# Kernel tuning notes

Measured on AMD Instinct MI355X. Metric: run time of the kernel, lower is better.

## Reference

```python
import jax, jax.numpy as jnp
import numpy as np

NEG_SLOPE = 0.2

def gat_conv(x, src, dst, n, W, a_src, a_dst, b):
    # PyG GATConv, heads=1: h = xW; e_ij = LeakyReLU(a_src.h_j + a_dst.h_i)
    # alpha = softmax over incoming edges of i; out_i = sum_j alpha_ij * h_j + b
    h = x @ W                               # [N, F_out]
    s_src = h @ a_src                       # [N]
    s_dst = h @ a_dst                       # [N]
    e = s_src[src] + s_dst[dst]             # [E]
    e = jnp.where(e > 0, e, NEG_SLOPE * e)  # leaky relu
    # numerically stable scatter-softmax over destination groups
    m = jax.ops.segment_max(e, dst, num_segments=n)          # [N]
    ee = jnp.exp(e - m[dst])                                  # [E]
    denom = jax.ops.segment_sum(ee, dst, num_segments=n)      # [N]
    alpha = ee / denom[dst]                                    # [E]
    out = jax.ops.segment_sum(alpha[:, None] * h[src], dst, num_segments=n)
    return out + b

def add_self_loops(edge_index, n):
    loops = jnp.arange(n, dtype=edge_index.dtype)
    src = jnp.concatenate([edge_index[0], loops])
    dst = jnp.concatenate([edge_index[1], loops])
    return src, dst

def setup_inputs() -> dict:
    key = jax.random.key(0)
    ks = jax.random.split(key, 12)
    N, E, F_IN, H1, H2, C = 50000, 800000, 1433, 512, 256, 7
    x = jax.random.normal(ks[0], (N, F_IN), dtype=jnp.float32)
    edge_index = jax.random.randint(ks[1], (2, E), 0, N, dtype=jnp.int64)
    def glorot(k, shape):
        lim = float(np.sqrt(6.0 / (shape[0] + shape[-1])))
        return jax.random.uniform(k, shape, jnp.float32, -lim, lim)
    params = {
        'W1': glorot(ks[2], (F_IN, H1)), 'as1': glorot(ks[3], (H1,)), 'ad1': glorot(ks[4], (H1,)), 'b1': jnp.zeros((H1,), jnp.float32),
        'W2': glorot(ks[5], (H1, H2)), 'as2': glorot(ks[6], (H2,)), 'ad2': glorot(ks[7], (H2,)), 'b2': jnp.zeros((H2,), jnp.float32),
        'W3': glorot(ks[8], (H2, C)), 'as3': glorot(ks[9], (C,)), 'ad3': glorot(ks[10], (C,)), 'b3': jnp.zeros((C,), jnp.float32),
    }
    return {'x': x, 'edge_index': edge_index, **params}

def reference(x, edge_index, W1, as1, ad1, b1, W2, as2, ad2, b2, W3, as3, ad3, b3):
    n = x.shape[0]
    src, dst = add_self_loops(edge_index, n)
    h = jax.nn.relu(gat_conv(x, src, dst, n, W1, as1, ad1, b1))
    h = jax.nn.relu(gat_conv(h, src, dst, n, W2, as2, ad2, b2))
    h = gat_conv(h, src, dst, n, W3, as3, ad3, b3)
    return jax.nn.log_softmax(h, axis=1)
```

## Files before the change

kernel.cpp:

```cpp
#include <hip/hip_runtime.h>
#include <hip/hip_bf16.h>
#include <math.h>

constexpr int N_NODES = 50000;
constexpr int E_EDGES = 800000;
constexpr int E_TOT   = E_EDGES + N_NODES;
constexpr int F_IN  = 1433;
constexpr int KPAD1 = 1440;
constexpr int F1 = 512;
constexpr int F2 = 256;
constexpr int NC = 7;
constexpr int MAXDEG = 1024;
constexpr float NEG_SLOPE = 0.2f;

typedef unsigned short u16;
typedef unsigned int   u32;
typedef short s16x8 __attribute__((ext_vector_type(8)));
typedef float f32x4 __attribute__((ext_vector_type(4)));
typedef float float4a __attribute__((ext_vector_type(4), aligned(4)));

__device__ inline u16 f2b(float f) {
    u32 u = __float_as_uint(f);
    u32 r = (u + 0x7fffu + ((u >> 16) & 1u)) >> 16;
    return (u16)r;
}
__device__ inline float b2f(u16 b) { return __uint_as_float(((u32)b) << 16); }

__device__ inline u32 pkbf16(float lo, float hi) {
    union { __hip_bfloat162 h; u32 u; } c;
    c.h = __float22bfloat162_rn(make_float2(lo, hi));
    return c.u;
}

__device__ inline void gload_lds16(const void* g, void* l) {
    __builtin_amdgcn_global_load_lds(
        (const __attribute__((address_space(1))) u32*)g,
        (__attribute__((address_space(3))) u32*)l, 16, 0, 0);
}

__device__ inline void loadA8(const float* p, int gk, float4a& v0, float4a& v1) {
    if (gk + 8 <= F_IN) {
        v0 = *(const float4a*)p;
        v1 = *(const float4a*)(p + 4);
    } else {
#pragma unroll
        for (int i = 0; i < 4; ++i) v0[i] = (gk + i < F_IN) ? p[i] : 0.f;
#pragma unroll
        for (int i = 0; i < 4; ++i) v1[i] = (gk + 4 + i < F_IN) ? p[4 + i] : 0.f;
    }
}

__global__ void count_dst_kernel(const int* __restrict__ dst, int* __restrict__ counts) {
    int i = blockIdx.x * blockDim.x + threadIdx.x;
    if (i < E_TOT) {
        int d = (i < E_EDGES) ? dst[i] : (i - E_EDGES);
        atomicAdd(&counts[d], 1);
    }
}

__global__ __launch_bounds__(1024) void scan_kernel(const int* __restrict__ counts,
                                                    int* __restrict__ row_ptr, int n) {
    __shared__ int part[1024];
    int t = threadIdx.x;
    int chunk = (n + 1023) / 1024;
    int lo = t * chunk;
    int hi = min(lo + chunk, n);
    int s = 0;
    for (int i = lo; i < hi; ++i) s += counts[i];
    part[t] = s;
    __syncthreads();
    for (int off = 1; off < 1024; off <<= 1) {
        int v = 0;
        if (t >= off) v = part[t - off];
        __syncthreads();
        part[t] += v;
        __syncthreads();
    }
    int run = part[t] - s;
    for (int i = lo; i < hi; ++i) { row_ptr[i] = run; run += counts[i]; }
    if (t == 1023) row_ptr[n] = part[1023];
}

__global__ void scatter_kernel(const int* __restrict__ src, const int* __restrict__ dst,
                               const int* __restrict__ row_ptr, int* __restrict__ fill,
                               int* __restrict__ col) {
    int i = blockIdx.x * blockDim.x + threadIdx.x;
    if (i < E_TOT) {
        int s = (i < E_EDGES) ? src[i] : (i - E_EDGES);
        int d = (i < E_EDGES) ? dst[i] : (i - E_EDGES);
        int p = row_ptr[d] + atomicAdd(&fill[d], 1);
        col[p] = s;
    }
}

__global__ void convert_wt_kernel(const float* __restrict__ W, u32* __restrict__ Wt,
                                  int K, int Nn, int KP) {
    int p = blockIdx.x * blockDim.x + threadIdx.x;
    int ppr = KP / 2;
    if (p >= Nn * ppr) return;
    int n = p / ppr;
    int k = (p - n * ppr) * 2;
    float v0 = (k + 0 < K) ? W[(size_t)(k + 0) * Nn + n] : 0.f;
    float v1 = (k + 1 < K) ? W[(size_t)(k + 1) * Nn + n] : 0.f;
    Wt[p] = (u32)f2b(v0) | ((u32)f2b(v1) << 16);
}

__global__ __launch_bounds__(256, 2) void gemm1_fused(const float* __restrict__ A,
                                                      const u16* __restrict__ Bt,
                                                      u16* __restrict__ C) {
    constexpr int M = N_NODES;
    constexpr int ABUF = 64 * 32;
    constexpr int BBUF = 512 * 32;
    __shared__ u16 sA[2 * ABUF];
    __shared__ u16 sB[2 * BBUF];
    int tid  = threadIdx.x;
    int wave = tid >> 6;
    int lane = tid & 63;
    int quad = lane >> 4;
    int lm   = lane & 15;
    int m0 = blockIdx.x * 64;

    int arow  = min(m0 + (tid >> 2), M - 1);
    int aslot = (tid & 3) ^ ((tid >> 3) & 3);
    const float* xcol = A + (size_t)arow * F_IN + aslot * 8;
    int acolbase = aslot * 8;

    const u16* gB[8];
    u16* lB[8];
#pragma unroll
    for (int c = 0; c < 8; ++c) {
        int chunk = wave * 8 + c;
        int row  = chunk * 16 + (lane >> 2);
        int slot = (lane & 3) ^ ((lane >> 3) & 3);
        gB[c] = Bt + (size_t)row * KPAD1 + slot * 8;
        lB[c] = &sB[chunk * 512];
    }

    f32x4 acc[4][8];
#pragma unroll
    for (int i = 0; i < 4; ++i)
#pragma unroll
        for (int j = 0; j < 8; ++j) acc[i][j] = (f32x4){0.f, 0.f, 0.f, 0.f};

    int rdoff = (quad ^ ((lm >> 1) & 3)) * 8;

    {
#pragma unroll
        for (int c = 0; c < 8; ++c) gload_lds16(gB[c], lB[c]);
        float4a a0, a1;
        loadA8(xcol, acolbase, a0, a1);
        uint4 pk;
        pk.x = pkbf16(a0[0], a0[1]); pk.y = pkbf16(a0[2], a0[3]);
        pk.z = pkbf16(a1[0], a1[1]); pk.w = pkbf16(a1[2], a1[3]);
        *(uint4*)&sA[tid * 8] = pk;
    }
    __syncthreads();

    int cur = 0;
    for (int k0 = 0; k0 < KPAD1; k0 += 32) {
        int kn = k0 + 32;
        bool hasnext = kn < KPAD1;
        int nxt = cur ^ 1;

        float4a a0, a1;
        if (hasnext) {
#pragma unroll
            for (int c = 0; c < 8; ++c) gload_lds16(gB[c] + kn, lB[c] + nxt * BBUF);
            loadA8(xcol + kn, acolbase + kn, a0, a1);
        }

        const u16* sAc = &sA[cur * ABUF];
        const u16* sBc = &sB[cur * BBUF];
        s16x8 af[4], bf[8];
#pragma unroll
        for (int mt = 0; mt < 4; ++mt)
            af[mt] = *(const s16x8*)&sAc[(mt * 16 + lm) * 32 + rdoff];
#pragma unroll
        for (int nt = 0; nt < 8; ++nt)
            bf[nt] = *(const s16x8*)&sBc[(wave * 128 + nt * 16 + lm) * 32 + rdoff];
#pragma unroll
        for (int mt = 0; mt < 4; ++mt)
#pragma unroll
            for (int nt = 0; nt < 8; ++nt)
                acc[mt][nt] = __builtin_amdgcn_mfma_f32_16x16x32_bf16(
                    af[mt], bf[nt], acc[mt][nt], 0, 0, 0);

        if (hasnext) {
            uint4 pk;
            pk.x = pkbf16(a0[0], a0[1]); pk.y = pkbf16(a0[2], a0[3]);
            pk.z = pkbf16(a1[0], a1[1]); pk.w = pkbf16(a1[2], a1[3]);
            *(uint4*)&sA[nxt * ABUF + tid * 8] = pk;
        }
        __syncthreads();
        cur = nxt;
    }

#pragma unroll
    for (int mt = 0; mt < 4; ++mt) {
        int mbase = m0 + mt * 16 + quad * 4;
#pragma unroll
        for (int nt = 0; nt < 8; ++nt) {
            int n = wave * 128 + nt * 16 + lm;
#pragma unroll
            for (int r = 0; r < 4; ++r) {
                int m = mbase + r;
                if (m < M) C[(size_t)m * F1 + n] = f2b(acc[mt][nt][r]);
            }
        }
    }
}

__global__ __launch_bounds__(256) void mfma_gemm_bt(const u16* __restrict__ A,
                                                    const u16* __restrict__ Bt,
                                                    u16* __restrict__ C,
                                                    int M, int N, int K) {
    __shared__ u16 sA[128 * 32];
    __shared__ u16 sB[128 * 32];
    int tid  = threadIdx.x;
    int wave = tid >> 6;
    int lane = tid & 63;
    int quad = lane >> 4;
    int lm   = lane & 15;
    int wm = wave & 1;
    int wn = wave >> 1;
    int m0 = blockIdx.y * 128;
    int n0 = blockIdx.x * 128;

    int ch0 = wave * 2, ch1 = wave * 2 + 1;
    int rsub = lane >> 2;
    int csub = (lane & 3) * 8;
    int ar0 = min(m0 + ch0 * 16 + rsub, M - 1);
    int ar1 = min(m0 + ch1 * 16 + rsub, M - 1);
    int br0 = n0 + ch0 * 16 + rsub;
    int br1 = n0 + ch1 * 16 + rsub;
    const u16* gA0 = A + (size_t)ar0 * K + csub;
    const u16* gA1 = A + (size_t)ar1 * K + csub;
    const u16* gB0 = Bt + (size_t)br0 * K + csub;
    const u16* gB1 = Bt + (size_t)br1 * K + csub;

    f32x4 acc[4][4];
#pragma unroll
    for (int i = 0; i < 4; ++i)
#pragma unroll
        for (int j = 0; j < 4; ++j) acc[i][j] = (f32x4){0.f, 0.f, 0.f, 0.f};

    for (int k0 = 0; k0 < K; k0 += 32) {
        gload_lds16(gA0 + k0, &sA[ch0 * 512]);
        gload_lds16(gA1 + k0, &sA[ch1 * 512]);
        gload_lds16(gB0 + k0, &sB[ch0 * 512]);
        gload_lds16(gB1 + k0, &sB[ch1 * 512]);
        __syncthreads();

        s16x8 af[4], bf[4];
#pragma unroll
        for (int mt = 0; mt < 4; ++mt)
            af[mt] = *(const s16x8*)&sA[(wm * 64 + mt * 16 + lm) * 32 + quad * 8];
#pragma unroll
        for (int nt = 0; nt < 4; ++nt)
            bf[nt] = *(const s16x8*)&sB[(wn * 64 + nt * 16 + lm) * 32 + quad * 8];
#pragma unroll
        for (int mt = 0; mt < 4; ++mt)
#pragma unroll
            for (int nt = 0; nt < 4; ++nt)
                acc[mt][nt] = __builtin_amdgcn_mfma_f32_16x16x32_bf16(
                    af[mt], bf[nt], acc[mt][nt], 0, 0, 0);
        __syncthreads();
    }

#pragma unroll
    for (int mt = 0; mt < 4; ++mt) {
        int mbase = m0 + wm * 64 + mt * 16 + quad * 4;
#pragma unroll
        for (int nt = 0; nt < 4; ++nt) {
            int n = n0 + wn * 64 + nt * 16 + lm;
#pragma unroll
            for (int r = 0; r < 4; ++r) {
                int m = mbase + r;
                if (m < M) C[(size_t)m * N + n] = f2b(acc[mt][nt][r]);
            }
        }
    }
}

template <int F>
__global__ __launch_bounds__(256) void scores_bf16_kernel(const u16* __restrict__ h,
                                                          const float* __restrict__ a_src,
                                                          const float* __restrict__ a_dst,
                                                          float* __restrict__ s_src,
                                                          float* __restrict__ s_dst, int n) {
    int gwid = (blockIdx.x * blockDim.x + threadIdx.x) >> 6;
    int lane = threadIdx.x & 63;
    if (gwid >= n) return;
    const u32* row = (const u32*)(h + (size_t)gwid * F);
    float acc1 = 0.f, acc2 = 0.f;
    for (int p = lane; p < F / 2; p += 64) {
        u32 u = row[p];
        float v0 = b2f((u16)(u & 0xffff));
        float v1 = b2f((u16)(u >> 16));
        acc1 += v0 * a_src[2 * p] + v1 * a_src[2 * p + 1];
        acc2 += v0 * a_dst[2 * p] + v1 * a_dst[2 * p + 1];
    }
#pragma unroll
    for (int o = 32; o; o >>= 1) {
        acc1 += __shfl_xor(acc1, o);
        acc2 += __shfl_xor(acc2, o);
    }
    if (lane == 0) { s_src[gwid] = acc1; s_dst[gwid] = acc2; }
}

template <int F>
__global__ __launch_bounds__(256) void scores_kernel(const float* __restrict__ h,
                                                     const float* __restrict__ a_src,
                                                     const float* __restrict__ a_dst,
                                                     float* __restrict__ s_src,
                                                     float* __restrict__ s_dst, int n) {
    int gwid = (blockIdx.x * blockDim.x + threadIdx.x) >> 6;
    int lane = threadIdx.x & 63;
    if (gwid >= n) return;
    const float* row = h + (size_t)gwid * F;
    float acc1 = 0.f, acc2 = 0.f;
    for (int f = lane; f < F; f += 64) {
        float v = row[f];
        acc1 += v * a_src[f];
        acc2 += v * a_dst[f];
    }
#pragma unroll
    for (int o = 32; o; o >>= 1) {
        acc1 += __shfl_xor(acc1, o);
        acc2 += __shfl_xor(acc2, o);
    }
    if (lane == 0) { s_src[gwid] = acc1; s_dst[gwid] = acc2; }
}

template <int F, bool OUT_BF16>
__global__ __launch_bounds__(256) void agg_gather_kernel(const u16* __restrict__ h,
                                                         const float* __restrict__ s_src,
                                                         const float* __restrict__ s_dst,
                                                         const float* __restrict__ bias,
                                                         const int* __restrict__ row_ptr,
                                                         const int* __restrict__ col,
                                                         void* __restrict__ out) {
    constexpr int UPL = F / 128;
    int node = blockIdx.x;
    int tid = threadIdx.x;
    int wave = tid >> 6;
    int lane = tid & 63;
    int beg = row_ptr[node];
    int deg = min(row_ptr[node + 1] - beg, MAXDEG);

    __shared__ float w[MAXDEG];
    __shared__ int cs[MAXDEG];
    __shared__ float sdenom;
    __shared__ float red[4][F];

    if (wave == 0) {
        float sd = s_dst[node];
        float m = -1e30f;
        for (int j = lane; j < deg; j += 64) {
            int s = col[beg + j];
            cs[j] = s;
            float e = s_src[s] + sd;
            e = (e > 0.f) ? e : NEG_SLOPE * e;
            w[j] = e;
            m = fmaxf(m, e);
        }
#pragma unroll
        for (int o = 32; o; o >>= 1) m = fmaxf(m, __shfl_xor(m, o));
        float sum = 0.f;
        for (int j = lane; j < deg; j += 64) {
            float v = expf(w[j] - m);
            w[j] = v;
            sum += v;
        }
#pragma unroll
        for (int o = 32; o; o >>= 1) sum += __shfl_xor(sum, o);
        if (lane == 0) sdenom = sum;
    }
    __syncthreads();
    float inv = 1.0f / sdenom;

    float acc[2 * UPL];
#pragma unroll
    for (int e = 0; e < 2 * UPL; ++e) acc[e] = 0.f;

    int j = wave;
    for (; j + 4 < deg; j += 8) {
        float wg0 = w[j] * inv;
        float wg1 = w[j + 4] * inv;
        const u32* r0 = (const u32*)(h + (size_t)cs[j] * F) + lane * UPL;
        const u32* r1 = (const u32*)(h + (size_t)cs[j + 4] * F) + lane * UPL;
        u32 v0[UPL], v1[UPL];
        if constexpr (UPL == 4) {
            uint4 q0 = *(const uint4*)r0; v0[0] = q0.x; v0[1] = q0.y; v0[2] = q0.z; v0[3] = q0.w;
            uint4 q1 = *(const uint4*)r1; v1[0] = q1.x; v1[1] = q1.y; v1[2] = q1.z; v1[3] = q1.w;
        } else {
            uint2 q0 = *(const uint2*)r0; v0[0] = q0.x; v0[1] = q0.y;
            uint2 q1 = *(const uint2*)r1; v1[0] = q1.x; v1[1] = q1.y;
        }
#pragma unroll
        for (int u = 0; u < UPL; ++u) {
            acc[2 * u]     += wg0 * b2f((u16)(v0[u] & 0xffff)) + wg1 * b2f((u16)(v1[u] & 0xffff));
            acc[2 * u + 1] += wg0 * b2f((u16)(v0[u] >> 16))    + wg1 * b2f((u16)(v1[u] >> 16));
        }
    }
    if (j < deg) {
        float wg = w[j] * inv;
        const u32* r = (const u32*)(h + (size_t)cs[j] * F) + lane * UPL;
        u32 v[UPL];
        if constexpr (UPL == 4) {
            uint4 q = *(const uint4*)r; v[0] = q.x; v[1] = q.y; v[2] = q.z; v[3] = q.w;
        } else {
            uint2 q = *(const uint2*)r; v[0] = q.x; v[1] = q.y;
        }
#pragma unroll
        for (int u = 0; u < UPL; ++u) {
            acc[2 * u]     += wg * b2f((u16)(v[u] & 0xffff));
            acc[2 * u + 1] += wg * b2f((u16)(v[u] >> 16));
        }
    }

#pragma unroll
    for (int e = 0; e < 2 * UPL; ++e) red[wave][lane * 2 * UPL + e] = acc[e];
    __syncthreads();

    if constexpr (OUT_BF16) {
        if (tid < F / 2) {
            int f = tid * 2;
            float v0 = red[0][f] + red[1][f] + red[2][f] + red[3][f] + bias[f];
            float v1 = red[0][f + 1] + red[1][f + 1] + red[2][f + 1] + red[3][f + 1] + bias[f + 1];
            v0 = fmaxf(v0, 0.f);
            v1 = fmaxf(v1, 0.f);
            ((u32*)out)[(size_t)node * (F / 2) + tid] = (u32)f2b(v0) | ((u32)f2b(v1) << 16);
        }
    } else {
        if (tid < F) {
            float v = red[0][tid] + red[1][tid] + red[2][tid] + red[3][tid] + bias[tid];
            ((float*)out)[(size_t)node * F + tid] = fmaxf(v, 0.f);
        }
    }
}

__global__ __launch_bounds__(64) void agg_lsm7_kernel(const float* __restrict__ h,
                                                      const float* __restrict__ s_src,
                                                      const float* __restrict__ s_dst,
                                                      const float* __restrict__ bias,
                                                      const int* __restrict__ row_ptr,
                                                      const int* __restrict__ col,
                                                      float* __restrict__ out) {
    int node = blockIdx.x;
    int lane = threadIdx.x;
    int beg = row_ptr[node];
    int deg = min(row_ptr[node + 1] - beg, MAXDEG);

    __shared__ float w[MAXDEG];
    __shared__ int cs[MAXDEG];

    float sd = s_dst[node];
    float m = -1e30f;
    for (int j = lane; j < deg; j += 64) {
        int s = col[beg + j];
        cs[j] = s;
        float e = s_src[s] + sd;
        e = (e > 0.f) ? e : NEG_SLOPE * e;
        w[j] = e;
        m = fmaxf(m, e);
    }
#pragma unroll
    for (int o = 32; o; o >>= 1) m = fmaxf(m, __shfl_xor(m, o));
    float sum = 0.f;
    for (int j = lane; j < deg; j += 64) {
        float v = expf(w[j] - m);
        w[j] = v;
        sum += v;
    }
#pragma unroll
    for (int o = 32; o; o >>= 1) sum += __shfl_xor(sum, o);
    float inv = 1.0f / sum;

    float a[NC];
#pragma unroll
    for (int f = 0; f < NC; ++f) a[f] = 0.f;
    for (int j = lane; j < deg; j += 64) {
        float wg = w[j] * inv;
        const float* row = h + (size_t)cs[j] * NC;
#pragma unroll
        for (int f = 0; f < NC; ++f) a[f] += wg * row[f];
    }
#pragma unroll
    for (int f = 0; f < NC; ++f)
#pragma unroll
        for (int o = 32; o; o >>= 1) a[f] += __shfl_xor(a[f], o);

    if (lane == 0) {
        float vals[NC];
        float mx = -1e30f;
#pragma unroll
        for (int f = 0; f < NC; ++f) { vals[f] = a[f] + bias[f]; mx = fmaxf(mx, vals[f]); }
        float ssum = 0.f;
#pragma unroll
        for (int f = 0; f < NC; ++f) ssum += expf(vals[f] - mx);
        float lse = mx + logf(ssum);
#pragma unroll
        for (int f = 0; f < NC; ++f) out[(size_t)node * NC + f] = vals[f] - lse;
    }
}

__global__ __launch_bounds__(256) void gemm3_kernel(const float* __restrict__ A,
                                                    const float* __restrict__ W,
                                                    float* __restrict__ out, int n) {
    __shared__ float sW[F2 * NC];
    for (int i = threadIdx.x; i < F2 * NC; i += blockDim.x) sW[i] = W[i];
    __syncthreads();
    int gwid = (blockIdx.x * blockDim.x + threadIdx.x) >> 6;
    int lane = threadIdx.x & 63;
    if (gwid >= n) return;
    const float* row = A + (size_t)gwid * F2;
    float4 v = *(const float4*)(row + lane * 4);
    float res = 0.f;
#pragma unroll
    for (int c = 0; c < NC; ++c) {
        float p = v.x * sW[(lane * 4 + 0) * NC + c] + v.y * sW[(lane * 4 + 1) * NC + c] +
                  v.z * sW[(lane * 4 + 2) * NC + c] + v.w * sW[(lane * 4 + 3) * NC + c];
#pragma unroll
        for (int o = 32; o; o >>= 1) p += __shfl_xor(p, o);
        if (lane == c) res = p;
    }
    if (lane < NC) out[(size_t)gwid * NC + lane] = res;
}

extern "C" void kernel_launch(void* const* d_in, const int* in_sizes, int n_in,
                              void* d_out, int out_size, void* d_ws, size_t ws_size,
                              hipStream_t stream) {
    const float* x   = (const float*)d_in[0];
    const int* ei    = (const int*)d_in[1];
    const int* src   = ei;
    const int* dst   = ei + E_EDGES;
    const float* W1  = (const float*)d_in[2];
    const float* as1 = (const float*)d_in[3];
    const float* ad1 = (const float*)d_in[4];
    const float* b1  = (const float*)d_in[5];
    const float* W2  = (const float*)d_in[6];
    const float* as2 = (const float*)d_in[7];
    const float* ad2 = (const float*)d_in[8];
    const float* b2  = (const float*)d_in[9];
    const float* W3  = (const float*)d_in[10];
    const float* as3 = (const float*)d_in[11];
    const float* ad3 = (const float*)d_in[12];
    const float* b3  = (const float*)d_in[13];
    float* outp = (float*)d_out;

    char* base = (char*)d_ws;
    u16*  a1b = (u16*)base;
    u16*  h2b = (u16*)(base + 51200000);
    float* a2 = (float*)(base + 76800000);
    float* h3 = (float*)(base + 128000000);
    u16*  h1b = (u16*)(base + 144000000);
    u16*  W1t = (u16*)(base + 195200000);
    u16*  W2t = (u16*)(base + 196674560);
    float* ssrc = (float*)(base + 196936704);
    float* sdst = (float*)(base + 197136704);
    int* row_ptr = (int*)(base + 197336704);
    int* counts  = (int*)(base + 197536708);
    int* fill    = (int*)(base + 197736708);
    int* col     = (int*)(base + 197936708);

    hipMemsetAsync(counts, 0, sizeof(int) * N_NODES, stream);
    hipMemsetAsync(fill, 0, sizeof(int) * N_NODES, stream);

    {
        int blk = 256;
        int grid = (E_TOT + blk - 1) / blk;
        count_dst_kernel<<<grid, blk, 0, stream>>>(dst, counts);
        scan_kernel<<<1, 1024, 0, stream>>>(counts, row_ptr, N_NODES);
        scatter_kernel<<<grid, blk, 0, stream>>>(src, dst, row_ptr, fill, col);
    }

    {
        int nw1 = F1 * (KPAD1 / 2);
        convert_wt_kernel<<<(nw1 + 255) / 256, 256, 0, stream>>>(W1, (u32*)W1t, F_IN, F1, KPAD1);
        int nw2 = F2 * (F1 / 2);
        convert_wt_kernel<<<(nw2 + 255) / 256, 256, 0, stream>>>(W2, (u32*)W2t, F1, F2, F1);
    }

    int waves_grid = (N_NODES + 3) / 4;
    int mblocks = (N_NODES + 127) / 128;

    {
        int grid1 = (N_NODES + 63) / 64;
        gemm1_fused<<<grid1, 256, 0, stream>>>(x, W1t, h1b);
        scores_bf16_kernel<F1><<<waves_grid, 256, 0, stream>>>(h1b, as1, ad1, ssrc, sdst, N_NODES);
        agg_gather_kernel<F1, true><<<N_NODES, 256, 0, stream>>>(
            h1b, ssrc, sdst, b1, row_ptr, col, a1b);
    }
    {
        dim3 grid(F2 / 128, mblocks);
        mfma_gemm_bt<<<grid, 256, 0, stream>>>(a1b, W2t, h2b, N_NODES, F2, F1);
        scores_bf16_kernel<F2><<<waves_grid, 256, 0, stream>>>(h2b, as2, ad2, ssrc, sdst, N_NODES);
        agg_gather_kernel<F2, false><<<N_NODES, 256, 0, stream>>>(
            h2b, ssrc, sdst, b2, row_ptr, col, a2);
    }
    {
        gemm3_kernel<<<waves_grid, 256, 0, stream>>>(a2, W3, h3, N_NODES);
        scores_kernel<NC><<<waves_grid, 256, 0, stream>>>(h3, as3, ad3, ssrc, sdst, N_NODES);
        agg_lsm7_kernel<<<N_NODES, 64, 0, stream>>>(
            h3, ssrc, sdst, b3, row_ptr, col, outp);
    }
}
```

Baseline: 1.042 ms.

## Deepen gemm1 prefetch pipeline, swizzle gemm2 LDS, one-wave online-softmax aggregation

Gemm1 now prefetches the A operand two k-steps ahead with explicit waitcnt control and raw barriers, unrolled by two, and peels the last k tiles so the bounds-checked tail load happens only once. The second GEMM gains the same XOR-swizzled LDS slot layout as gemm1 to cut bank conflicts. The aggregation kernels for layers one and two switch from one 256-thread block per node (two softmax passes plus an LDS reduction) to one wave per node with a single-pass online softmax that rescales the accumulator as it goes. The trade-offs are more expf calls per edge, serial edge processing within each wave, and hand-written waitcnt counts that could be wrong.

```diff
diff --git a/kernel.cpp b/kernel.cpp
--- a/kernel.cpp
+++ b/kernel.cpp
@@ -36,18 +36,6 @@
     __builtin_amdgcn_global_load_lds(
         (const __attribute__((address_space(1))) u32*)g,
         (__attribute__((address_space(3))) u32*)l, 16, 0, 0);
-}
-
-__device__ inline void loadA8(const float* p, int gk, float4a& v0, float4a& v1) {
-    if (gk + 8 <= F_IN) {
-        v0 = *(const float4a*)p;
-        v1 = *(const float4a*)(p + 4);
-    } else {
-#pragma unroll
-        for (int i = 0; i < 4; ++i) v0[i] = (gk + i < F_IN) ? p[i] : 0.f;
-#pragma unroll
-        for (int i = 0; i < 4; ++i) v1[i] = (gk + 4 + i < F_IN) ? p[4 + i] : 0.f;
-    }
 }
 
 __global__ void count_dst_kernel(const int* __restrict__ dst, int* __restrict__ counts) {
@@ -105,6 +93,45 @@
     Wt[p] = (u32)f2b(v0) | ((u32)f2b(v1) << 16);
 }
 
+#define GEMM1_COMPUTE(P)                                                        \
+    {                                                                           \
+        const u16* sAc = &sA[(P) * ABUF];                                       \
+        const u16* sBc = &sB[(P) * BBUF];                                       \
+        s16x8 af[4], bf[8];                                                     \
+        _Pragma("unroll")                                                       \
+        for (int mt = 0; mt < 4; ++mt)                                          \
+            af[mt] = *(const s16x8*)&sAc[(mt * 16 + lm) * 32 + rdoff];          \
+        _Pragma("unroll")                                                       \
+        for (int nt = 0; nt < 8; ++nt)                                          \
+            bf[nt] = *(const s16x8*)&sBc[(wave * 128 + nt * 16 + lm) * 32 + rdoff]; \
+        _Pragma("unroll")                                                       \
+        for (int mt = 0; mt < 4; ++mt)                                          \
+            _Pragma("unroll")                                                   \
+            for (int nt = 0; nt < 8; ++nt)                                      \
+                acc[mt][nt] = __builtin_amdgcn_mfma_f32_16x16x32_bf16(          \
+                    af[mt], bf[nt], acc[mt][nt], 0, 0, 0);                      \
+    }
+
+#define GEMM1_BODY(i, P, Q)                                                     \
+    {                                                                           \
+        __builtin_amdgcn_s_barrier();                                           \
+        int kA = ((i) + 2) * 32;                                                \
+        aR0[P] = *(const float4a*)(xcol + kA);                                  \
+        aR1[P] = *(const float4a*)(xcol + kA + 4);                              \
+        int kB = ((i) + 1) * 32;                                                \
+        _Pragma("unroll")                                                       \
+        for (int c = 0; c < 8; ++c) gload_lds16(gB[c] + kB, lB[c] + (Q) * BBUF);\
+        asm volatile("s_waitcnt vmcnt(10)" ::: "memory");                       \
+        GEMM1_COMPUTE(P);                                                       \
+        uint4 pk_;                                                              \
+        pk_.x = pkbf16(aR0[Q][0], aR0[Q][1]);                                   \
+        pk_.y = pkbf16(aR0[Q][2], aR0[Q][3]);                                   \
+        pk_.z = pkbf16(aR1[Q][0], aR1[Q][1]);                                   \
+        pk_.w = pkbf16(aR1[Q][2], aR1[Q][3]);                                   \
+        *(uint4*)&sA[(Q) * ABUF + tid * 8] = pk_;                               \
+        asm volatile("s_waitcnt lgkmcnt(0)" ::: "memory");                      \
+    }
+
 __global__ __launch_bounds__(256, 2) void gemm1_fused(const float* __restrict__ A,
                                                       const u16* __restrict__ Bt,
                                                       u16* __restrict__ C) {
@@ -123,7 +150,6 @@
     int arow  = min(m0 + (tid >> 2), M - 1);
     int aslot = (tid & 3) ^ ((tid >> 3) & 3);
     const float* xcol = A + (size_t)arow * F_IN + aslot * 8;
-    int acolbase = aslot * 8;
 
     const u16* gB[8];
     u16* lB[8];
@@ -144,56 +170,63 @@
 
     int rdoff = (quad ^ ((lm >> 1) & 3)) * 8;
 
-    {
-#pragma unroll
-        for (int c = 0; c < 8; ++c) gload_lds16(gB[c], lB[c]);
-        float4a a0, a1;
-        loadA8(xcol, acolbase, a0, a1);
-        uint4 pk;
-        pk.x = pkbf16(a0[0], a0[1]); pk.y = pkbf16(a0[2], a0[3]);
-        pk.z = pkbf16(a1[0], a1[1]); pk.w = pkbf16(a1[2], a1[3]);
-        *(uint4*)&sA[tid * 8] = pk;
-    }
+    float4a aR0[2], aR1[2];
+
+    aR0[0] = *(const float4a*)(xcol + 0);
+    aR1[0] = *(const float4a*)(xcol + 4);
+    aR0[1] = *(const float4a*)(xcol + 32);
+    aR1[1] = *(const float4a*)(xcol + 36);
+#pragma unroll
+    for (int c = 0; c < 8; ++c) gload_lds16(gB[c], lB[c]);
+    asm volatile("s_waitcnt vmcnt(10)" ::: "memory");
+    {
+        uint4 pk_;
+        pk_.x = pkbf16(aR0[0][0], aR0[0][1]);
+        pk_.y = pkbf16(aR0[0][2], aR0[0][3]);
+        pk_.z = pkbf16(aR1[0][0], aR1[0][1]);
+        pk_.w = pkbf16(aR1[0][2], aR1[0][3]);
+        *(uint4*)&sA[tid * 8] = pk_;
+    }
+    asm volatile("s_waitcnt lgkmcnt(0)" ::: "memory");
+
+    for (int ii = 0; ii < 42; ii += 2) {
+        GEMM1_BODY(ii, 0, 1);
+        GEMM1_BODY(ii + 1, 1, 0);
+    }
+
     __syncthreads();
-
-    int cur = 0;
-    for (int k0 = 0; k0 < KPAD1; k0 += 32) {
-        int kn = k0 + 32;
-        bool hasnext = kn < KPAD1;
-        int nxt = cur ^ 1;
-
-        float4a a0, a1;
-        if (hasnext) {
-#pragma unroll
-            for (int c = 0; c < 8; ++c) gload_lds16(gB[c] + kn, lB[c] + nxt * BBUF);
-            loadA8(xcol + kn, acolbase + kn, a0, a1);
-        }
-
-        const u16* sAc = &sA[cur * ABUF];
-        const u16* sBc = &sB[cur * BBUF];
-        s16x8 af[4], bf[8];
-#pragma unroll
-        for (int mt = 0; mt < 4; ++mt)
-            af[mt] = *(const s16x8*)&sAc[(mt * 16 + lm) * 32 + rdoff];
-#pragma unroll
-        for (int nt = 0; nt < 8; ++nt)
-            bf[nt] = *(const s16x8*)&sBc[(wave * 128 + nt * 16 + lm) * 32 + rdoff];
-#pragma unroll
-        for (int mt = 0; mt < 4; ++mt)
-#pragma unroll
-            for (int nt = 0; nt < 8; ++nt)
-                acc[mt][nt] = __builtin_amdgcn_mfma_f32_16x16x32_bf16(
-                    af[mt], bf[nt], acc[mt][nt], 0, 0, 0);
-
-        if (hasnext) {
-            uint4 pk;
-            pk.x = pkbf16(a0[0], a0[1]); pk.y = pkbf16(a0[2], a0[3]);
-            pk.z = pkbf16(a1[0], a1[1]); pk.w = pkbf16(a1[2], a1[3]);
-            *(uint4*)&sA[nxt * ABUF + tid * 8] = pk;
-        }
-        __syncthreads();
-        cur = nxt;
-    }
+    float tv[8];
+    {
+        int c0 = 1408 + aslot * 8;
+#pragma unroll
+        for (int q = 0; q < 8; ++q)
+            tv[q] = (c0 + q < F_IN) ? xcol[1408 + q] : 0.f;
+    }
+#pragma unroll
+    for (int c = 0; c < 8; ++c) gload_lds16(gB[c] + 43 * 32, lB[c] + BBUF);
+    GEMM1_COMPUTE(0);
+    {
+        uint4 pk_;
+        pk_.x = pkbf16(aR0[1][0], aR0[1][1]);
+        pk_.y = pkbf16(aR0[1][2], aR0[1][3]);
+        pk_.z = pkbf16(aR1[1][0], aR1[1][1]);
+        pk_.w = pkbf16(aR1[1][2], aR1[1][3]);
+        *(uint4*)&sA[ABUF + tid * 8] = pk_;
+    }
+    __syncthreads();
+#pragma unroll
+    for (int c = 0; c < 8; ++c) gload_lds16(gB[c] + 44 * 32, lB[c]);
+    GEMM1_COMPUTE(1);
+    {
+        uint4 pk_;
+        pk_.x = pkbf16(tv[0], tv[1]);
+        pk_.y = pkbf16(tv[2], tv[3]);
+        pk_.z = pkbf16(tv[4], tv[5]);
+        pk_.w = pkbf16(tv[6], tv[7]);
+        *(uint4*)&sA[tid * 8] = pk_;
+    }
+    __syncthreads();
+    GEMM1_COMPUTE(0);
 
 #pragma unroll
     for (int mt = 0; mt < 4; ++mt) {
@@ -228,7 +261,8 @@
 
     int ch0 = wave * 2, ch1 = wave * 2 + 1;
     int rsub = lane >> 2;
-    int csub = (lane & 3) * 8;
+    int slot = (lane & 3) ^ ((lane >> 3) & 3);
+    int csub = slot * 8;
     int ar0 = min(m0 + ch0 * 16 + rsub, M - 1);
     int ar1 = min(m0 + ch1 * 16 + rsub, M - 1);
     int br0 = n0 + ch0 * 16 + rsub;
@@ -244,6 +278,8 @@
 #pragma unroll
         for (int j = 0; j < 4; ++j) acc[i][j] = (f32x4){0.f, 0.f, 0.f, 0.f};
 
+    int rdoff = (quad ^ ((lm >> 1) & 3)) * 8;
+
     for (int k0 = 0; k0 < K; k0 += 32) {
         gload_lds16(gA0 + k0, &sA[ch0 * 512]);
         gload_lds16(gA1 + k0, &sA[ch1 * 512]);
@@ -254,10 +290,10 @@
         s16x8 af[4], bf[4];
 #pragma unroll
         for (int mt = 0; mt < 4; ++mt)
-            af[mt] = *(const s16x8*)&sA[(wm * 64 + mt * 16 + lm) * 32 + quad * 8];
+            af[mt] = *(const s16x8*)&sA[(wm * 64 + mt * 16 + lm) * 32 + rdoff];
 #pragma unroll
         for (int nt = 0; nt < 4; ++nt)
-            bf[nt] = *(const s16x8*)&sB[(wn * 64 + nt * 16 + lm) * 32 + quad * 8];
+            bf[nt] = *(const s16x8*)&sB[(wn * 64 + nt * 16 + lm) * 32 + rdoff];
 #pragma unroll
         for (int mt = 0; mt < 4; ++mt)
 #pragma unroll
@@ -333,110 +369,103 @@
 }
 
 template <int F, bool OUT_BF16>
-__global__ __launch_bounds__(256) void agg_gather_kernel(const u16* __restrict__ h,
-                                                         const float* __restrict__ s_src,
-                                                         const float* __restrict__ s_dst,
-                                                         const float* __restrict__ bias,
-                                                         const int* __restrict__ row_ptr,
-                                                         const int* __restrict__ col,
-                                                         void* __restrict__ out) {
+__global__ __launch_bounds__(256) void agg_online_kernel(
+        const u16* __restrict__ h, const float* __restrict__ s_src,
+        const float* __restrict__ s_dst, const float* __restrict__ bias,
+        const int* __restrict__ row_ptr, const int* __restrict__ col,
+        void* __restrict__ out, int n) {
     constexpr int UPL = F / 128;
-    int node = blockIdx.x;
-    int tid = threadIdx.x;
-    int wave = tid >> 6;
-    int lane = tid & 63;
-    int beg = row_ptr[node];
-    int deg = min(row_ptr[node + 1] - beg, MAXDEG);
-
-    __shared__ float w[MAXDEG];
-    __shared__ int cs[MAXDEG];
-    __shared__ float sdenom;
-    __shared__ float red[4][F];
-
-    if (wave == 0) {
-        float sd = s_dst[node];
-        float m = -1e30f;
-        for (int j = lane; j < deg; j += 64) {
-            int s = col[beg + j];
-            cs[j] = s;
-            float e = s_src[s] + sd;
-            e = (e > 0.f) ? e : NEG_SLOPE * e;
-            w[j] = e;
-            m = fmaxf(m, e);
-        }
-#pragma unroll
-        for (int o = 32; o; o >>= 1) m = fmaxf(m, __shfl_xor(m, o));
-        float sum = 0.f;
-        for (int j = lane; j < deg; j += 64) {
-            float v = expf(w[j] - m);
-            w[j] = v;
-            sum += v;
-        }
-#pragma unroll
-        for (int o = 32; o; o >>= 1) sum += __shfl_xor(sum, o);
-        if (lane == 0) sdenom = sum;
-    }
-    __syncthreads();
-    float inv = 1.0f / sdenom;
-
+    int gwid = (blockIdx.x * blockDim.x + threadIdx.x) >> 6;
+    int lane = threadIdx.x & 63;
+    if (gwid >= n) return;
+    int beg = row_ptr[gwid];
+    int end = row_ptr[gwid + 1];
+    float sd = s_dst[gwid];
+    const u32* hw = (const u32*)h;
+    int loff = lane * UPL;
+
+    float m = -1e30f, denom = 0.f;
     float acc[2 * UPL];
 #pragma unroll
     for (int e = 0; e < 2 * UPL; ++e) acc[e] = 0.f;
 
-    int j = wave;
-    for (; j + 4 < deg; j += 8) {
-        float wg0 = w[j] * inv;
-        float wg1 = w[j + 4] * inv;
-        const u32* r0 = (const u32*)(h + (size_t)cs[j] * F) + lane * UPL;
-        const u32* r1 = (const u32*)(h + (size_t)cs[j + 4] * F) + lane * UPL;
+    int j = beg;
+    for (; j + 2 <= end; j += 2) {
+        int c0 = col[j], c1 = col[j + 1];
+        const u32* r0 = hw + (size_t)c0 * (F / 2) + loff;
+        const u32* r1 = hw + (size_t)c1 * (F / 2) + loff;
         u32 v0[UPL], v1[UPL];
         if constexpr (UPL == 4) {
-            uint4 q0 = *(const uint4*)r0; v0[0] = q0.x; v0[1] = q0.y; v0[2] = q0.z; v0[3] = q0.w;
-            uint4 q1 = *(const uint4*)r1; v1[0] = q1.x; v1[1] = q1.y; v1[2] = q1.z; v1[3] = q1.w;
+            uint4 q0 = *(const uint4*)r0; v0[0]=q0.x; v0[1]=q0.y; v0[2]=q0.z; v0[3]=q0.w;
+            uint4 q1 = *(const uint4*)r1; v1[0]=q1.x; v1[1]=q1.y; v1[2]=q1.z; v1[3]=q1.w;
         } else {
-            uint2 q0 = *(const uint2*)r0; v0[0] = q0.x; v0[1] = q0.y;
-            uint2 q1 = *(const uint2*)r1; v1[0] = q1.x; v1[1] = q1.y;
-        }
+            uint2 q0 = *(const uint2*)r0; v0[0]=q0.x; v0[1]=q0.y;
+            uint2 q1 = *(const uint2*)r1; v1[0]=q1.x; v1[1]=q1.y;
+        }
+        float e0 = s_src[c0] + sd; e0 = (e0 > 0.f) ? e0 : NEG_SLOPE * e0;
+        float e1 = s_src[c1] + sd; e1 = (e1 > 0.f) ? e1 : NEG_SLOPE * e1;
+        float mn = fmaxf(fmaxf(m, e0), e1);
+        float sc = expf(m - mn);
+        float w0 = expf(e0 - mn);
+        float w1 = expf(e1 - mn);
+        denom = denom * sc + w0 + w1;
+        m = mn;
 #pragma unroll
         for (int u = 0; u < UPL; ++u) {
-            acc[2 * u]     += wg0 * b2f((u16)(v0[u] & 0xffff)) + wg1 * b2f((u16)(v1[u] & 0xffff));
-            acc[2 * u + 1] += wg0 * b2f((u16)(v0[u] >> 16))    + wg1 * b2f((u16)(v1[u] >> 16));
-        }
-    }
-    if (j < deg) {
-        float wg = w[j] * inv;
-        const u32* r = (const u32*)(h + (size_t)cs[j] * F) + lane * UPL;
-        u32 v[UPL];
+            acc[2*u]   = acc[2*u]   * sc + w0 * b2f((u16)(v0[u] & 0xffff))
+                                         + w1 * b2f((u16)(v1[u] & 0xffff));
+            acc[2*u+1] = acc[2*u+1] * sc + w0 * b2f((u16)(v0[u] >> 16))
+                                         + w1 * b2f((u16)(v1[u] >> 16));
+        }
+    }
+    if (j < end) {
+        int c0 = col[j];
+        const u32* r0 = hw + (size_t)c0 * (F / 2) + loff;
+        u32 v0[UPL];
         if constexpr (UPL == 4) {
-            uint4 q = *(const uint4*)r; v[0] = q.x; v[1] = q.y; v[2] = q.z; v[3] = q.w;
+            uint4 q0 = *(const uint4*)r0; v0[0]=q0.x; v0[1]=q0.y; v0[2]=q0.z; v0[3]=q0.w;
         } else {
-            uint2 q = *(const uint2*)r; v[0] = q.x; v[1] = q.y;
-        }
+            uint2 q0 = *(const uint2*)r0; v0[0]=q0.x; v0[1]=q0.y;
+        }
+        float e0 = s_src[c0] + sd; e0 = (e0 > 0.f) ? e0 : NEG_SLOPE * e0;
+        float mn = fmaxf(m, e0);
+        float sc = expf(m - mn);
+        float w0 = expf(e0 - mn);
+        denom = denom * sc + w0;
+        m = mn;
 #pragma unroll
         for (int u = 0; u < UPL; ++u) {
-            acc[2 * u]     += wg * b2f((u16)(v[u] & 0xffff));
-            acc[2 * u + 1] += wg * b2f((u16)(v[u] >> 16));
-        }
-    }
-
-#pragma unroll
-    for (int e = 0; e < 2 * UPL; ++e) red[wave][lane * 2 * UPL + e] = acc[e];
-    __syncthreads();
-
+            acc[2*u]   = acc[2*u]   * sc + w0 * b2f((u16)(v0[u] & 0xffff));
+            acc[2*u+1] = acc[2*u+1] * sc + w0 * b2f((u16)(v0[u] >> 16));
+        }
+    }
+
+    float inv = 1.0f / denom;
     if constexpr (OUT_BF16) {
-        if (tid < F / 2) {
-            int f = tid * 2;
-            float v0 = red[0][f] + red[1][f] + red[2][f] + red[3][f] + bias[f];
-            float v1 = red[0][f + 1] + red[1][f + 1] + red[2][f + 1] + red[3][f + 1] + bias[f + 1];
-            v0 = fmaxf(v0, 0.f);
-            v1 = fmaxf(v1, 0.f);
-            ((u32*)out)[(size_t)node * (F / 2) + tid] = (u32)f2b(v0) | ((u32)f2b(v1) << 16);
+        const float2* bp2 = (const float2*)bias;
+        u32 ov[UPL];
+#pragma unroll
+        for (int u = 0; u < UPL; ++u) {
+            float2 bb = bp2[loff + u];
+            float v0 = fmaxf(acc[2*u]   * inv + bb.x, 0.f);
+            float v1 = fmaxf(acc[2*u+1] * inv + bb.y, 0.f);
+            ov[u] = pkbf16(v0, v1);
+        }
+        u32* op = (u32*)out + (size_t)gwid * (F / 2) + loff;
+        if constexpr (UPL == 4) {
+            uint4 q = {ov[0], ov[1], ov[2], ov[3]};
+            *(uint4*)op = q;
+        } else {
+            uint2 q = {ov[0], ov[1]};
+            *(uint2*)op = q;
         }
     } else {
-        if (tid < F) {
-            float v = red[0][tid] + red[1][tid] + red[2][tid] + red[3][tid] + bias[tid];
-            ((float*)out)[(size_t)node * F + tid] = fmaxf(v, 0.f);
-        }
+        const float* bp = bias + 2 * loff;
+        float4 q = { fmaxf(acc[0] * inv + bp[0], 0.f),
+                     fmaxf(acc[1] * inv + bp[1], 0.f),
+                     fmaxf(acc[2] * inv + bp[2], 0.f),
+                     fmaxf(acc[3] * inv + bp[3], 0.f) };
+        *(float4*)((float*)out + (size_t)gwid * F + 2 * loff) = q;
     }
 }
 
@@ -589,15 +618,15 @@
         int grid1 = (N_NODES + 63) / 64;
         gemm1_fused<<<grid1, 256, 0, stream>>>(x, W1t, h1b);
         scores_bf16_kernel<F1><<<waves_grid, 256, 0, stream>>>(h1b, as1, ad1, ssrc, sdst, N_NODES);
-        agg_gather_kernel<F1, true><<<N_NODES, 256, 0, stream>>>(
-            h1b, ssrc, sdst, b1, row_ptr, col, a1b);
+        agg_online_kernel<F1, true><<<waves_grid, 256, 0, stream>>>(
+            h1b, ssrc, sdst, b1, row_ptr, col, a1b, N_NODES);
     }
     {
         dim3 grid(F2 / 128, mblocks);
         mfma_gemm_bt<<<grid, 256, 0, stream>>>(a1b, W2t, h2b, N_NODES, F2, F1);
         scores_bf16_kernel<F2><<<waves_grid, 256, 0, stream>>>(h2b, as2, ad2, ssrc, sdst, N_NODES);
-        agg_gather_kernel<F2, false><<<N_NODES, 256, 0, stream>>>(
-            h2b, ssrc, sdst, b2, row_ptr, col, a2);
+        agg_online_kernel<F2, false><<<waves_grid, 256, 0, stream>>>(
+            h2b, ssrc, sdst, b2, row_ptr, col, a2, N_NODES);
     }
     {
         gemm3_kernel<<<waves_grid, 256, 0, stream>>>(a2, W3, h3, N_NODES);
```

Result: no change. 1.039 ms (-0.3%).
